# Kernel tuning notes

Measured on AMD Instinct MI355X. Metric: run time of the kernel, lower is better.

## Reference

```python
import jax, jax.numpy as jnp
import numpy as np

IN_DIM, OUT_DIM = 64, 64
HIDDEN = [64, 64, 64]
D = IN_DIM * OUT_DIM  # number of independent per-edge small MLPs
B = 256


def setup_inputs() -> dict:
    key = jax.random.key(0)
    ks = jax.random.split(key, 10)

    def kaiming(k, shape, fan_in):
        # kaiming_uniform_ with a=0, nonlinearity='relu': bound = sqrt(6/fan_in)
        bound = np.sqrt(6.0 / fan_in)
        return jax.random.uniform(k, shape, jnp.float32, -bound, bound)

    def bias_init(k, shape, fan_in):
        bound = 1.0 / np.sqrt(fan_in)
        return jax.random.uniform(k, shape, jnp.float32, -bound, bound)

    h0, h1, h2 = HIDDEN
    inp = {
        "x": jax.random.normal(ks[0], (B, IN_DIM), jnp.float32),
        # Input_Linear: weight (out_dim, in_dim, h0); fan_in per torch kaiming on this tensor is in_dim*h0,
        # bias uses reset_parameters(1) -> fan_in=1
        "w0": kaiming(ks[1], (OUT_DIM, IN_DIM, h0), IN_DIM * h0),
        "b0": bias_init(ks[2], (D, h0), 1),
        # Linear(d, o=h1, i=h0): weight (d, h1, h0); kaiming fan_in = h0 (last dim), bias fan_in = i = h0
        "w1": kaiming(ks[3], (D, h1, h0), h0),
        "b1": bias_init(ks[4], (D, h1), h0),
        "w2": kaiming(ks[5], (D, h2, h1), h1),
        "b2": bias_init(ks[6], (D, h2), h1),
        # Output_Linear: weight (out_dim, in_dim*h2), fan_in = in_dim*h2
        "wout": kaiming(ks[7], (OUT_DIM, IN_DIM * h2), IN_DIM * h2),
        "bout": bias_init(ks[8], (OUT_DIM,), IN_DIM * h2),
    }
    return inp


def reference(x, w0, b0, w1, b1, w2, b2, wout, bout):
    Bsz = x.shape[0]
    # Input_Linear: broadcast outer product -> (B, out_dim, in_dim, h0) -> (B, d, h0)
    out = x[:, None, :, None] * w0[None, :, :, :]
    out = out.reshape(Bsz, D, HIDDEN[0]) + b0[None, :, :]
    out = jax.nn.relu(out)
    # Hidden per-edge Linear layers: 'doi,Bdi->Bdo'
    out = jnp.einsum('doi,bdi->bdo', w1, out) + b1[None, :, :]
    out = jax.nn.relu(out)
    out = jnp.einsum('doi,bdi->bdo', w2, out) + b2[None, :, :]
    out = jax.nn.relu(out)
    # Output_Linear: (B, d, h2) -> (B, out_dim, in_dim*h2); 'oi,boi->bo'
    xv = out.reshape(Bsz, OUT_DIM, IN_DIM * HIDDEN[-1])
    return jnp.einsum('oi,boi->bo', wout, xv) + bout[None, :]
```

## Files before the change

kernel.cpp:

```cpp
#include <hip/hip_runtime.h>
#include <hip/hip_bf16.h>


#define D_EDGES 4096

typedef __attribute__((ext_vector_type(4))) float f32x4;
typedef __attribute__((ext_vector_type(8))) short bf16x8;

__device__ __forceinline__ unsigned pk2(float a, float b) {
    __hip_bfloat162 h = __float22bfloat162_rn(float2{a, b});
    return *reinterpret_cast<unsigned*>(&h);
}

union BFr { unsigned u[4]; bf16x8 v; };

__global__ __launch_bounds__(256, 4) void kan_mfma(
    const float* __restrict__ x,
    const float* __restrict__ w0g,
    const float* __restrict__ b0g,
    const float* __restrict__ w1g,
    const float* __restrict__ b1g,
    const float* __restrict__ w2g,
    const float* __restrict__ b2g,
    const float* __restrict__ woutg,
    float* __restrict__ outbuf,
    int atomic_mode)
{
    const int d = blockIdx.x, o = d >> 6, ii = d & 63;
    const int t = threadIdx.x;
    const int lane = t & 63, wv = t >> 6;

    __shared__ __align__(16) unsigned char W1s[64 * 128];
    __shared__ __align__(16) unsigned char W2s[64 * 128];
    __shared__ __align__(16) unsigned char Hs[4 * 16 * 128];
    __shared__ __align__(16) float sx[256];
    __shared__ __align__(16) float sw0[64], sb0[64], sb1[64], sb2[64], swo[64];

    {
        const int orow = t >> 2, q = t & 3;
        const unsigned swz  = (unsigned)((orow & 7) << 4);
        const unsigned base = (unsigned)(orow * 128);
        const float* s1 = w1g + (size_t)d * 4096 + orow * 64 + q * 16;
        const float* s2 = w2g + (size_t)d * 4096 + orow * 64 + q * 16;

        float4 a0 = ((const float4*)s1)[0], a1 = ((const float4*)s1)[1];
        float4 a2 = ((const float4*)s1)[2], a3 = ((const float4*)s1)[3];
        uint4 u0 = { pk2(a0.x, a0.y), pk2(a0.z, a0.w), pk2(a1.x, a1.y), pk2(a1.z, a1.w) };
        uint4 u1 = { pk2(a2.x, a2.y), pk2(a2.z, a2.w), pk2(a3.x, a3.y), pk2(a3.z, a3.w) };
        *(uint4*)&W1s[base + ((unsigned)(q * 32)      ^ swz)] = u0;
        *(uint4*)&W1s[base + ((unsigned)(q * 32 + 16) ^ swz)] = u1;

        a0 = ((const float4*)s2)[0]; a1 = ((const float4*)s2)[1];
        a2 = ((const float4*)s2)[2]; a3 = ((const float4*)s2)[3];
        uint4 v0 = { pk2(a0.x, a0.y), pk2(a0.z, a0.w), pk2(a1.x, a1.y), pk2(a1.z, a1.w) };
        uint4 v1 = { pk2(a2.x, a2.y), pk2(a2.z, a2.w), pk2(a3.x, a3.y), pk2(a3.z, a3.w) };
        *(uint4*)&W2s[base + ((unsigned)(q * 32)      ^ swz)] = v0;
        *(uint4*)&W2s[base + ((unsigned)(q * 32 + 16) ^ swz)] = v1;
    }
    sx[t] = x[t * 64 + ii];
    if (t < 64) {
        sw0[t] = w0g[(size_t)d * 64 + t];
        sb0[t] = b0g[(size_t)d * 64 + t];
        sb1[t] = b1g[(size_t)d * 64 + t];
        sb2[t] = b2g[(size_t)d * 64 + t];
        swo[t] = woutg[(size_t)o * 4096 + ii * 64 + t];
    }
    __syncthreads();

    const int arow = lane & 15;
    const int kb   = (lane >> 4) * 16;
    const int g8   = (lane >> 4) * 8;
    const unsigned lswz = (unsigned)((lane & 7) << 4);
    const int r0 = (lane >> 4) * 4;
    const unsigned hbase = (unsigned)(wv * 2048 + arow * 128);
    const unsigned hswz  = (unsigned)((arow & 7) << 4);
    const f32x4 zero4 = { 0.f, 0.f, 0.f, 0.f };

    bf16x8 wf1[4][2];
#pragma unroll
    for (int nt = 0; nt < 4; ++nt)
#pragma unroll
        for (int ks = 0; ks < 2; ++ks)
            wf1[nt][ks] = *(const bf16x8*)&W1s[(nt * 16 + arow) * 128 +
                            ((unsigned)(ks * 64 + kb) ^ lswz)];

    float4 w0v[2][2], b0v[2][2];
#pragma unroll
    for (int ks = 0; ks < 2; ++ks) {
        const int k0 = ks * 32 + g8;
        w0v[ks][0] = *(const float4*)&sw0[k0];
        w0v[ks][1] = *(const float4*)&sw0[k0 + 4];
        b0v[ks][0] = *(const float4*)&sb0[k0];
        b0v[ks][1] = *(const float4*)&sb0[k0 + 4];
    }

#pragma unroll
    for (int mti = 0; mti < 4; ++mti) {
        const float xm = sx[wv * 64 + mti * 16 + arow];

        f32x4 a1[4] = { zero4, zero4, zero4, zero4 };
#pragma unroll
        for (int ks = 0; ks < 2; ++ks) {
            float4 wa = w0v[ks][0], wb = w0v[ks][1];
            float4 ba = b0v[ks][0], bb = b0v[ks][1];
            float v0 = fmaxf(fmaf(xm, wa.x, ba.x), 0.f);
            float v1 = fmaxf(fmaf(xm, wa.y, ba.y), 0.f);
            float v2 = fmaxf(fmaf(xm, wa.z, ba.z), 0.f);
            float v3 = fmaxf(fmaf(xm, wa.w, ba.w), 0.f);
            float v4 = fmaxf(fmaf(xm, wb.x, bb.x), 0.f);
            float v5 = fmaxf(fmaf(xm, wb.y, bb.y), 0.f);
            float v6 = fmaxf(fmaf(xm, wb.z, bb.z), 0.f);
            float v7 = fmaxf(fmaf(xm, wb.w, bb.w), 0.f);
            BFr bh;
            bh.u[0] = pk2(v0, v1); bh.u[1] = pk2(v2, v3);
            bh.u[2] = pk2(v4, v5); bh.u[3] = pk2(v6, v7);
#pragma unroll
            for (int nt = 0; nt < 4; ++nt)
                a1[nt] = __builtin_amdgcn_mfma_f32_16x16x32_bf16(
                    wf1[nt][ks], bh.v, a1[nt], 0, 0, 0);
        }

#pragma unroll
        for (int nt = 0; nt < 4; ++nt) {
            float4 bv = *(const float4*)&sb1[nt * 16 + r0];
            float v0 = fmaxf(a1[nt][0] + bv.x, 0.f);
            float v1 = fmaxf(a1[nt][1] + bv.y, 0.f);
            float v2 = fmaxf(a1[nt][2] + bv.z, 0.f);
            float v3 = fmaxf(a1[nt][3] + bv.w, 0.f);
            uint2 hp = { pk2(v0, v1), pk2(v2, v3) };
            *(uint2*)&Hs[hbase + ((unsigned)(2 * (nt * 16 + r0)) ^ hswz)] = hp;
        }

        f32x4 a2[4] = { zero4, zero4, zero4, zero4 };
#pragma unroll
        for (int ks = 0; ks < 2; ++ks) {
            bf16x8 bh2 = *(const bf16x8*)&Hs[hbase + ((unsigned)(ks * 64 + kb) ^ hswz)];
#pragma unroll
            for (int nt = 0; nt < 4; ++nt) {
                bf16x8 wf2f = *(const bf16x8*)&W2s[(nt * 16 + arow) * 128 +
                                ((unsigned)(ks * 64 + kb) ^ lswz)];
                a2[nt] = __builtin_amdgcn_mfma_f32_16x16x32_bf16(
                    wf2f, bh2, a2[nt], 0, 0, 0);
            }
        }

        float p = 0.f;
#pragma unroll
        for (int nt = 0; nt < 4; ++nt) {
            float4 bv = *(const float4*)&sb2[nt * 16 + r0];
            float4 wo = *(const float4*)&swo[nt * 16 + r0];
            p = fmaf(fmaxf(a2[nt][0] + bv.x, 0.f), wo.x, p);
            p = fmaf(fmaxf(a2[nt][1] + bv.y, 0.f), wo.y, p);
            p = fmaf(fmaxf(a2[nt][2] + bv.z, 0.f), wo.z, p);
            p = fmaf(fmaxf(a2[nt][3] + bv.w, 0.f), wo.w, p);
        }
        p += __shfl_xor(p, 16);
        p += __shfl_xor(p, 32);
        const int b = wv * 64 + mti * 16 + arow;
        if (lane < 16) {
            if (atomic_mode) atomicAdd(&outbuf[b * 64 + o], p);
            else             outbuf[(size_t)d * 256 + b] = p;
        }
    }
}

__global__ __launch_bounds__(256) void kan_reduce(
    const float* __restrict__ partial,
    const float* __restrict__ bout,
    float* __restrict__ y)
{
    const int o = blockIdx.x;
    const int b = threadIdx.x;
    float acc = bout[o];
    const float* p = partial + (size_t)o * (64 * 256) + b;
#pragma unroll
    for (int i = 0; i < 64; ++i)
        acc += p[i * 256];
    y[b * 64 + o] = acc;
}

__global__ __launch_bounds__(256) void kan_init_out(const float* __restrict__ bout,
                                                    float* __restrict__ y)
{
    const int idx = blockIdx.x * 256 + threadIdx.x;
    y[idx] = bout[idx & 63];
}

extern "C" void kernel_launch(void* const* d_in, const int* in_sizes, int n_in,
                              void* d_out, int out_size, void* d_ws, size_t ws_size,
                              hipStream_t stream) {
    const float* x    = (const float*)d_in[0];
    const float* w0   = (const float*)d_in[1];
    const float* b0   = (const float*)d_in[2];
    const float* w1   = (const float*)d_in[3];
    const float* b1   = (const float*)d_in[4];
    const float* w2   = (const float*)d_in[5];
    const float* b2   = (const float*)d_in[6];
    const float* wout = (const float*)d_in[7];
    const float* bout = (const float*)d_in[8];
    float* y = (float*)d_out;

    const size_t partial_bytes = (size_t)D_EDGES * 256 * sizeof(float);

    if (ws_size >= partial_bytes) {
        float* partial = (float*)d_ws;
        kan_mfma<<<D_EDGES, 256, 0, stream>>>(x, w0, b0, w1, b1, w2, b2, wout, partial, 0);
        kan_reduce<<<64, 256, 0, stream>>>(partial, bout, y);
    } else {
        kan_init_out<<<64, 256, 0, stream>>>(bout, y);
        kan_mfma<<<D_EDGES, 256, 0, stream>>>(x, w0, b0, w1, b1, w2, b2, wout, y, 1);
    }
}
```

Measured before the change: 42.67 us.

## Permute W1 rows so layer-1 MFMA output feeds layer-2 directly in registers

W1 rows are stored in LDS under a bit permutation, so each lane's layer-1 MFMA accumulator already holds the K-slice layout that layer 2 expects as its B operand. This removes the LDS round trip through the Hs buffer for hidden activations. W2 fragments are now loaded into registers once per block instead of on every m-tile. In exchange, register pressure rises with eight more bf16x8 fragments per lane under launch_bounds(256,4), and the bias indexing must match the permutation exactly.

```diff
diff --git a/kernel.cpp b/kernel.cpp
--- a/kernel.cpp
+++ b/kernel.cpp
@@ -10,6 +10,10 @@
 __device__ __forceinline__ unsigned pk2(float a, float b) {
     __hip_bfloat162 h = __float22bfloat162_rn(float2{a, b});
     return *reinterpret_cast<unsigned*>(&h);
+}
+
+__device__ __forceinline__ int rho(int n) {
+    return (n & 0x23) | ((n & 0x18) >> 1) | ((n & 0x04) << 2);
 }
 
 union BFr { unsigned u[4]; bf16x8 v; };
@@ -32,14 +36,16 @@
 
     __shared__ __align__(16) unsigned char W1s[64 * 128];
     __shared__ __align__(16) unsigned char W2s[64 * 128];
-    __shared__ __align__(16) unsigned char Hs[4 * 16 * 128];
     __shared__ __align__(16) float sx[256];
     __shared__ __align__(16) float sw0[64], sb0[64], sb1[64], sb2[64], swo[64];
 
     {
         const int orow = t >> 2, q = t & 3;
-        const unsigned swz  = (unsigned)((orow & 7) << 4);
-        const unsigned base = (unsigned)(orow * 128);
+        const int prow = rho(orow);
+        const unsigned swz1  = (unsigned)((prow & 7) << 4);
+        const unsigned base1 = (unsigned)(prow * 128);
+        const unsigned swz2  = (unsigned)((orow & 7) << 4);
+        const unsigned base2 = (unsigned)(orow * 128);
         const float* s1 = w1g + (size_t)d * 4096 + orow * 64 + q * 16;
         const float* s2 = w2g + (size_t)d * 4096 + orow * 64 + q * 16;
 
@@ -47,15 +53,15 @@
         float4 a2 = ((const float4*)s1)[2], a3 = ((const float4*)s1)[3];
         uint4 u0 = { pk2(a0.x, a0.y), pk2(a0.z, a0.w), pk2(a1.x, a1.y), pk2(a1.z, a1.w) };
         uint4 u1 = { pk2(a2.x, a2.y), pk2(a2.z, a2.w), pk2(a3.x, a3.y), pk2(a3.z, a3.w) };
-        *(uint4*)&W1s[base + ((unsigned)(q * 32)      ^ swz)] = u0;
-        *(uint4*)&W1s[base + ((unsigned)(q * 32 + 16) ^ swz)] = u1;
+        *(uint4*)&W1s[base1 + ((unsigned)(q * 32)      ^ swz1)] = u0;
+        *(uint4*)&W1s[base1 + ((unsigned)(q * 32 + 16) ^ swz1)] = u1;
 
         a0 = ((const float4*)s2)[0]; a1 = ((const float4*)s2)[1];
         a2 = ((const float4*)s2)[2]; a3 = ((const float4*)s2)[3];
         uint4 v0 = { pk2(a0.x, a0.y), pk2(a0.z, a0.w), pk2(a1.x, a1.y), pk2(a1.z, a1.w) };
         uint4 v1 = { pk2(a2.x, a2.y), pk2(a2.z, a2.w), pk2(a3.x, a3.y), pk2(a3.z, a3.w) };
-        *(uint4*)&W2s[base + ((unsigned)(q * 32)      ^ swz)] = v0;
-        *(uint4*)&W2s[base + ((unsigned)(q * 32 + 16) ^ swz)] = v1;
+        *(uint4*)&W2s[base2 + ((unsigned)(q * 32)      ^ swz2)] = v0;
+        *(uint4*)&W2s[base2 + ((unsigned)(q * 32 + 16) ^ swz2)] = v1;
     }
     sx[t] = x[t * 64 + ii];
     if (t < 64) {
@@ -72,17 +78,18 @@
     const int g8   = (lane >> 4) * 8;
     const unsigned lswz = (unsigned)((lane & 7) << 4);
     const int r0 = (lane >> 4) * 4;
-    const unsigned hbase = (unsigned)(wv * 2048 + arow * 128);
-    const unsigned hswz  = (unsigned)((arow & 7) << 4);
     const f32x4 zero4 = { 0.f, 0.f, 0.f, 0.f };
 
-    bf16x8 wf1[4][2];
+    bf16x8 wf1[4][2], wf2[4][2];
 #pragma unroll
     for (int nt = 0; nt < 4; ++nt)
 #pragma unroll
-        for (int ks = 0; ks < 2; ++ks)
+        for (int ks = 0; ks < 2; ++ks) {
             wf1[nt][ks] = *(const bf16x8*)&W1s[(nt * 16 + arow) * 128 +
                             ((unsigned)(ks * 64 + kb) ^ lswz)];
+            wf2[nt][ks] = *(const bf16x8*)&W2s[(nt * 16 + arow) * 128 +
+                            ((unsigned)(ks * 64 + kb) ^ lswz)];
+        }
 
     float4 w0v[2][2], b0v[2][2];
 #pragma unroll
@@ -120,28 +127,29 @@
                     wf1[nt][ks], bh.v, a1[nt], 0, 0, 0);
         }
 
+        unsigned pu[4][2];
 #pragma unroll
         for (int nt = 0; nt < 4; ++nt) {
-            float4 bv = *(const float4*)&sb1[nt * 16 + r0];
+            const int bb = ((nt >> 1) << 5) + ((nt & 1) << 2) + g8;
+            float4 bv = *(const float4*)&sb1[bb];
             float v0 = fmaxf(a1[nt][0] + bv.x, 0.f);
             float v1 = fmaxf(a1[nt][1] + bv.y, 0.f);
             float v2 = fmaxf(a1[nt][2] + bv.z, 0.f);
             float v3 = fmaxf(a1[nt][3] + bv.w, 0.f);
-            uint2 hp = { pk2(v0, v1), pk2(v2, v3) };
-            *(uint2*)&Hs[hbase + ((unsigned)(2 * (nt * 16 + r0)) ^ hswz)] = hp;
-        }
+            pu[nt][0] = pk2(v0, v1);
+            pu[nt][1] = pk2(v2, v3);
+        }
+        BFr f0, f1;
+        f0.u[0] = pu[0][0]; f0.u[1] = pu[0][1]; f0.u[2] = pu[1][0]; f0.u[3] = pu[1][1];
+        f1.u[0] = pu[2][0]; f1.u[1] = pu[2][1]; f1.u[2] = pu[3][0]; f1.u[3] = pu[3][1];
 
         f32x4 a2[4] = { zero4, zero4, zero4, zero4 };
 #pragma unroll
-        for (int ks = 0; ks < 2; ++ks) {
-            bf16x8 bh2 = *(const bf16x8*)&Hs[hbase + ((unsigned)(ks * 64 + kb) ^ hswz)];
-#pragma unroll
-            for (int nt = 0; nt < 4; ++nt) {
-                bf16x8 wf2f = *(const bf16x8*)&W2s[(nt * 16 + arow) * 128 +
-                                ((unsigned)(ks * 64 + kb) ^ lswz)];
-                a2[nt] = __builtin_amdgcn_mfma_f32_16x16x32_bf16(
-                    wf2f, bh2, a2[nt], 0, 0, 0);
-            }
+        for (int nt = 0; nt < 4; ++nt) {
+            a2[nt] = __builtin_amdgcn_mfma_f32_16x16x32_bf16(
+                wf2[nt][0], f0.v, a2[nt], 0, 0, 0);
+            a2[nt] = __builtin_amdgcn_mfma_f32_16x16x32_bf16(
+                wf2[nt][1], f1.v, a2[nt], 0, 0, 0);
         }
 
         float p = 0.f;
```

Measured after the change: 45.27 us. +6.1%, slower.
